# Performance work log

Hardware: AMD Instinct MI355X
Metric: run time of the kernel (lower is better)

## Reference

```python
import jax, jax.numpy as jnp
import numpy as np

K = 10          # hardcoded in module (self.K = 10)
H = 26          # neighbors per query point in this run
PAD_H = 28      # layer_ind2neighbor[layer_ind=0]
KP_EXTENT = 1.2 # linear-influence extent


def setup_inputs() -> dict:
    key = jax.random.key(0)
    ks = jax.random.split(key, 6)
    N, Ns, Cin, Cout = 65536, 65536, 64, 128
    q_pts = jax.random.normal(ks[0], (N, 3), jnp.float32)
    s_pts = jax.random.normal(ks[1], (Ns, 3), jnp.float32)
    neighb_inds = jax.random.randint(ks[2], (N, H), 0, Ns)
    x = jax.random.normal(ks[3], (Ns, Cin), jnp.float32)
    # kernel_points_generator: Linear(PAD_H*3 -> K*3)
    gen_W = jax.random.normal(ks[4], (K * 3, PAD_H * 3), jnp.float32) * (1.0 / np.sqrt(PAD_H * 3))
    gen_b = jnp.zeros((K * 3,), jnp.float32)
    # KPConv weights: [K, in, out] (kaiming_uniform in torch; scaled normal here)
    weights = jax.random.normal(ks[5], (K, Cin, Cout), jnp.float32) * (1.0 / np.sqrt(Cin))
    return {"q_pts": q_pts, "s_pts": s_pts, "x": x,
            "gen_W": gen_W, "gen_b": gen_b, "weights": weights,
            "neighb_inds": neighb_inds}


def _kpconv(q_pts, s_pts, x, gen_W, gen_b, weights, neighb_inds):
    N = q_pts.shape[0]
    # shadow support point far away (index Ns)
    s_pad = jnp.concatenate([s_pts, jnp.full((1, 3), 1e6, s_pts.dtype)], axis=0)
    neighbors = s_pad[neighb_inds] - q_pts[:, None, :]                          # [N,H,3]
    # generative kernel points: pad neighbor list with -1 up to PAD_H, run linear
    padded = jnp.concatenate(
        [neighbors, jnp.full((N, PAD_H - H, 3), -1.0, neighbors.dtype)], axis=1)
    kp = (padded.reshape(N, -1) @ gen_W.T + gen_b).reshape(N, 1, K, 3)          # [N,1,K,3]
    diff = neighbors[:, :, None, :] - kp                                        # [N,H,K,3]
    sq_d = jnp.sum(diff * diff, axis=3)                                         # [N,H,K]
    # KP_influence == 'linear'
    all_w = jnp.maximum(1.0 - jnp.sqrt(sq_d) / KP_EXTENT, 0.0)
    all_w = jnp.swapaxes(all_w, 1, 2)                                           # [N,K,H]
    # shadow feature row (zeros) at index Ns
    x_pad = jnp.concatenate([x, jnp.zeros((1, x.shape[1]), x.dtype)], axis=0)
    neighb_x = x_pad[neighb_inds]                                               # [N,H,Cin]
    weighted = jnp.einsum('nkh,nhi->nki', all_w, neighb_x)                      # [N,K,Cin]
    return jnp.einsum('nki,kio->no', weighted, weights)                         # [N,Cout]


def reference(q_pts, s_pts, x, gen_W, gen_b, weights, neighb_inds):
    return _kpconv(q_pts, s_pts, x, gen_W, gen_b, weights, neighb_inds)
```

## Files before the change

### kernel.cpp

```cpp
#include <hip/hip_runtime.h>
#include <stdint.h>

#define N_Q   65536
#define N_S   65536
#define NB_H  26
#define PAD_H 28
#define KP    10
#define CIN   64
#define COUT  128
#define MT    16
#define BM    16

typedef unsigned short u16x8  __attribute__((ext_vector_type(8)));
typedef float          f32x4  __attribute__((ext_vector_type(4)));
typedef _Float16       f16x8  __attribute__((ext_vector_type(8)));
typedef _Float16       f16x2  __attribute__((ext_vector_type(2)));
typedef unsigned int   u32x4  __attribute__((ext_vector_type(4)));
typedef unsigned int   u32x2  __attribute__((ext_vector_type(2)));

#define CVT_BLOCKS 2049
#define PACK_BLOCKS 40

static __device__ __forceinline__ unsigned short f2h(float f) {
  return __builtin_bit_cast(unsigned short, (_Float16)f);
}

static __device__ __forceinline__ unsigned int pkrtz_u32(float a, float b) {
  return __builtin_bit_cast(unsigned int, __builtin_amdgcn_cvt_pkrtz(a, b));
}

static __device__ __forceinline__ float fdot2u(unsigned int a, unsigned int b, float c) {
#if __has_builtin(__builtin_amdgcn_fdot2)
  return __builtin_amdgcn_fdot2(__builtin_bit_cast(f16x2, a),
                                __builtin_bit_cast(f16x2, b), c, false);
#else
  f16x2 ha = __builtin_bit_cast(f16x2, a), hb = __builtin_bit_cast(f16x2, b);
  return c + (float)ha[0] * (float)hb[0] + (float)ha[1] * (float)hb[1];
#endif
}

__global__ void prep_kernel(const float* __restrict__ x,
                            const float* __restrict__ w,
                            unsigned short* __restrict__ xh,
                            unsigned short* __restrict__ bp) {
  if (blockIdx.x < CVT_BLOCKS) {
    long t = (long)blockIdx.x * blockDim.x + threadIdx.x;
    long off = t * 8;
    if (off >= (long)(N_S + 1) * CIN) return;
    u16x8 o;
    if (off < (long)N_S * CIN) {
      f32x4 a = *(const f32x4*)(x + off);
      f32x4 b = *(const f32x4*)(x + off + 4);
      o[0] = f2h(a[0]); o[1] = f2h(a[1]); o[2] = f2h(a[2]); o[3] = f2h(a[3]);
      o[4] = f2h(b[0]); o[5] = f2h(b[1]); o[6] = f2h(b[2]); o[7] = f2h(b[3]);
    } else {
      o = (u16x8)0;
    }
    *(u16x8*)(xh + off) = o;
  } else {
    int t = (blockIdx.x - CVT_BLOCKS) * blockDim.x + threadIdx.x;
    if (t >= 8 * 20 * 64) return;
    int lane = t & 63;
    int frag = t >> 6;
    int ks = frag % 20;
    int ct = frag / 20;
    int row0 = ks * 32 + (lane >> 4) * 8;
    int col  = ct * 16 + (lane & 15);
    u16x8 o;
    #pragma unroll
    for (int j = 0; j < 8; ++j) o[j] = f2h(w[(row0 + j) * COUT + col]);
    *(u16x8*)(bp + (long)t * 8) = o;
  }
}

#define NBR(m, c)    (((float*)smem)[(m) * 80 + (c)])
#define KPQ(m, r)    (((float*)(smem + 5120))[(m) * 30 + (r)])
#define AW(m, hp, k) (((unsigned int*)(smem + 20480))[((m) * 13 + (hp)) * 12 + (k)])
#define INDX(m, h)   (((int*)(smem + 30464))[(m) * 26 + (h)])

__global__ void __launch_bounds__(256, 5)
kpconv_fused(const float* __restrict__ q_pts, const float* __restrict__ s_pts,
             const float* __restrict__ gen_W, const float* __restrict__ gen_b,
             const int* __restrict__ inds, const unsigned short* __restrict__ xh,
             const unsigned short* __restrict__ bp, float* __restrict__ out) {

  __shared__ char smem[32128] __attribute__((aligned(16)));
  unsigned short* sA = (unsigned short*)smem;

  const int  tid  = threadIdx.x;
  const int  lane = tid & 63;
  const int  wv   = tid >> 6;
  const int  m0   = wv * 4;
  const long row0 = (long)blockIdx.x * BM;

  #pragma unroll
  for (int it = 0; it < 2; ++it) {
    int idx = it * 64 + lane;
    if (idx < 4 * NB_H) {
      int m = m0 + idx / NB_H;
      int h = idx % NB_H;
      int n = (int)row0 + m;
      int ind = inds[n * NB_H + h];
      INDX(m, h) = ind;
      float sx, sy, sz;
      if ((unsigned)ind < (unsigned)N_S) {
        sx = s_pts[ind * 3 + 0]; sy = s_pts[ind * 3 + 1]; sz = s_pts[ind * 3 + 2];
      } else {
        sx = 1e6f; sy = 1e6f; sz = 1e6f;
      }
      NBR(m, h * 3 + 0) = sx - q_pts[n * 3 + 0];
      NBR(m, h * 3 + 1) = sy - q_pts[n * 3 + 1];
      NBR(m, h * 3 + 2) = sz - q_pts[n * 3 + 2];
    }
  }
  if (lane < 8) NBR(m0 + (lane >> 1), 78 + (lane & 1)) = -1.0f;
  asm volatile("s_waitcnt lgkmcnt(0)" ::: "memory");

  const int il = lane & 31;
  const int g2 = lane >> 5;
  const int i0 = il * 2;
  const int rA = m0 + g2, rB = m0 + 2 + g2;

  unsigned int xrA[NB_H];
  #pragma unroll
  for (int h = 0; h < NB_H; ++h)
    xrA[h] = *(const unsigned int*)(xh + (long)INDX(rA, h) * CIN + i0);

  #pragma unroll
  for (int it = 0; it < 2; ++it) {
    int idx = it * 64 + lane;
    if (idx < 4 * 30) {
      int m = m0 + idx / 30;
      int r = idx % 30;
      const float* Wr = gen_W + r * (PAD_H * 3);
      const f32x4* W4 = (const f32x4*)Wr;
      const f32x4* N4 = (const f32x4*)&NBR(m, 0);
      f32x4 accv = {0.f, 0.f, 0.f, 0.f};
      #pragma unroll
      for (int j = 0; j < 20; ++j) accv += W4[j] * N4[j];
      KPQ(m, r) = gen_b[r] - (Wr[80] + Wr[81] + Wr[82] + Wr[83])
                + accv[0] + accv[1] + accv[2] + accv[3];
    }
  }
  asm volatile("s_waitcnt lgkmcnt(0)" ::: "memory");

  for (int it = 0; it < 9; ++it) {
    int idx = it * 64 + lane;
    if (idx < 4 * 13 * KP) {
      int k  = idx % KP;
      int t  = idx / KP;
      int m  = m0 + (t & 3);
      int hp = t >> 2;
      float kx = KPQ(m, k * 3 + 0), ky = KPQ(m, k * 3 + 1), kz = KPQ(m, k * 3 + 2);
      int h0 = hp * 2;
      float dx0 = NBR(m, h0 * 3 + 0) - kx;
      float dy0 = NBR(m, h0 * 3 + 1) - ky;
      float dz0 = NBR(m, h0 * 3 + 2) - kz;
      float w0 = fmaxf(1.0f - sqrtf(dx0 * dx0 + dy0 * dy0 + dz0 * dz0) * (1.0f / 1.2f), 0.0f);
      float dx1 = NBR(m, h0 * 3 + 3) - kx;
      float dy1 = NBR(m, h0 * 3 + 4) - ky;
      float dz1 = NBR(m, h0 * 3 + 5) - kz;
      float w1 = fmaxf(1.0f - sqrtf(dx1 * dx1 + dy1 * dy1 + dz1 * dz1) * (1.0f / 1.2f), 0.0f);
      AW(m, hp, k) = pkrtz_u32(w0, w1);
    }
  }
  asm volatile("s_waitcnt lgkmcnt(0)" ::: "memory");
  __builtin_amdgcn_s_barrier();
  asm volatile("" ::: "memory");

  unsigned int xrB[NB_H];
  #pragma unroll
  for (int h = 0; h < NB_H; ++h)
    xrB[h] = *(const unsigned int*)(xh + (long)INDX(rB, h) * CIN + i0);

  const int kq  = (il & 15) >> 2;
  const int qhi = il >> 4;
  const int j2  = (2 * il) & 7;
  const int swz = (kq << 3) ^ (qhi << 5);

#define ROW_COMPUTE(RR, XR)                                                   \
  {                                                                           \
    float acc0[KP], acc1[KP];                                                 \
    _Pragma("unroll")                                                         \
    for (int k = 0; k < KP; ++k) { acc0[k] = 0.f; acc1[k] = 0.f; }            \
    _Pragma("unroll")                                                         \
    for (int p = 0; p < 13; ++p) {                                            \
      unsigned int r0 = XR[2 * p], r1 = XR[2 * p + 1];                        \
      unsigned int p0 = __builtin_amdgcn_perm(r1, r0, 0x05040100u);           \
      unsigned int p1 = __builtin_amdgcn_perm(r1, r0, 0x07060302u);           \
      unsigned int wr[KP];                                                    \
      *(u32x4*)&wr[0] = *(const u32x4*)&AW(RR, p, 0);                         \
      *(u32x4*)&wr[4] = *(const u32x4*)&AW(RR, p, 4);                         \
      *(u32x2*)&wr[8] = *(const u32x2*)&AW(RR, p, 8);                         \
      _Pragma("unroll")                                                       \
      for (int k = 0; k < KP; ++k) {                                          \
        acc0[k] = fdot2u(wr[k], p0, acc0[k]);                                 \
        acc1[k] = fdot2u(wr[k], p1, acc1[k]);                                 \
      }                                                                       \
    }                                                                         \
    const int hb = (((kq * 16 + (RR)) * 8 + j2) ^ swz) + qhi * 512;           \
    _Pragma("unroll")                                                         \
    for (int k = 0; k < KP; ++k)                                              \
      *(unsigned int*)(sA + k * 1024 + hb) = pkrtz_u32(acc0[k], acc1[k]);     \
  }

  ROW_COMPUTE(rA, xrA)
  ROW_COMPUTE(rB, xrB)
#undef ROW_COMPUTE

  const int ct0 = wv * 2, ct1 = ct0 + 1;
  u16x8 pb0[4], pb1[4];
  #pragma unroll
  for (int d = 0; d < 4; ++d) {
    pb0[d] = *(const u16x8*)(bp + (long)((ct0 * 20 + d) * 64 + lane) * 8);
    pb1[d] = *(const u16x8*)(bp + (long)((ct1 * 20 + d) * 64 + lane) * 8);
  }

  asm volatile("s_waitcnt lgkmcnt(0)" ::: "memory");
  __builtin_amdgcn_s_barrier();
  asm volatile("" ::: "memory");

  {
    const int a0 = (lane * 8) ^ ((lane >> 4) << 3);

    f32x4 acc[2];
    acc[0] = (f32x4){0.f, 0.f, 0.f, 0.f};
    acc[1] = (f32x4){0.f, 0.f, 0.f, 0.f};

    #pragma unroll
    for (int ks = 0; ks < 20; ++ks) {
      f16x8 b0 = __builtin_bit_cast(f16x8, pb0[ks & 3]);
      f16x8 b1 = __builtin_bit_cast(f16x8, pb1[ks & 3]);
      if (ks + 4 < 20) {
        pb0[ks & 3] = *(const u16x8*)(bp + (long)((ct0 * 20 + ks + 4) * 64 + lane) * 8);
        pb1[ks & 3] = *(const u16x8*)(bp + (long)((ct1 * 20 + ks + 4) * 64 + lane) * 8);
      }
      u16x8 au = *(const u16x8*)&sA[ks * 512 + (a0 ^ ((ks & 1) << 5))];
      f16x8 a = __builtin_bit_cast(f16x8, au);
      acc[0] = __builtin_amdgcn_mfma_f32_16x16x32_f16(a, b0, acc[0], 0, 0, 0);
      acc[1] = __builtin_amdgcn_mfma_f32_16x16x32_f16(a, b1, acc[1], 0, 0, 0);
    }

    const int col   = lane & 15;
    const int rbase = (lane >> 4) * 4;
    #pragma unroll
    for (int r = 0; r < 4; ++r) {
      long row = row0 + rbase + r;
      __builtin_nontemporal_store(acc[0][r], &out[row * COUT + ct0 * 16 + col]);
      __builtin_nontemporal_store(acc[1][r], &out[row * COUT + ct1 * 16 + col]);
    }
  }
}

extern "C" void kernel_launch(void* const* d_in, const int* in_sizes, int n_in,
                              void* d_out, int out_size, void* d_ws, size_t ws_size,
                              hipStream_t stream) {
  const float* q_pts = (const float*)d_in[0];
  const float* s_pts = (const float*)d_in[1];
  const float* x     = (const float*)d_in[2];
  const float* gen_W = (const float*)d_in[3];
  const float* gen_b = (const float*)d_in[4];
  const float* wts   = (const float*)d_in[5];
  const int*   inds  = (const int*)d_in[6];
  float* out = (float*)d_out;

  unsigned short* xh = (unsigned short*)d_ws;
  unsigned short* bp = xh + (size_t)(N_S + 1) * CIN;

  prep_kernel<<<CVT_BLOCKS + PACK_BLOCKS, 256, 0, stream>>>(x, wts, xh, bp);
  kpconv_fused<<<N_Q / BM, 256, 0, stream>>>(q_pts, s_pts, gen_W, gen_b,
                                             inds, xh, bp, out);
}
```

Baseline: 184.1 us.

## Stream neighbor feature gathers through an 8-slot register ring, interleaving both rows

Before, all 26 neighbor feature words for row A were gathered before the kernel-point stage, and all 26 for row B after the barrier. Now only the first 8 per row are prefetched, and the rest are loaded inside the weighted-sum loop through a rotating 8-entry register buffer. Rows A and B are also computed together in one loop. The aim is to cut register pressure and raise occupancy while overlapping gather latency with the dot-product work. The cost is that loads now sit closer to their use, which can expose memory latency, and the doubled accumulators for the two rows add registers of their own.

```diff
diff --git a/kernel.cpp b/kernel.cpp
--- a/kernel.cpp
+++ b/kernel.cpp
@@ -120,11 +120,12 @@
   const int g2 = lane >> 5;
   const int i0 = il * 2;
   const int rA = m0 + g2, rB = m0 + 2 + g2;
-
-  unsigned int xrA[NB_H];
-  #pragma unroll
-  for (int h = 0; h < NB_H; ++h)
+  unsigned int xrA[8], xrB[8];
+  #pragma unroll
+  for (int h = 0; h < 8; ++h) {
     xrA[h] = *(const unsigned int*)(xh + (long)INDX(rA, h) * CIN + i0);
+    xrB[h] = *(const unsigned int*)(xh + (long)INDX(rB, h) * CIN + i0);
+  }
 
   #pragma unroll
   for (int it = 0; it < 2; ++it) {
@@ -168,45 +169,57 @@
   __builtin_amdgcn_s_barrier();
   asm volatile("" ::: "memory");
 
-  unsigned int xrB[NB_H];
-  #pragma unroll
-  for (int h = 0; h < NB_H; ++h)
-    xrB[h] = *(const unsigned int*)(xh + (long)INDX(rB, h) * CIN + i0);
-
-  const int kq  = (il & 15) >> 2;
-  const int qhi = il >> 4;
-  const int j2  = (2 * il) & 7;
-  const int swz = (kq << 3) ^ (qhi << 5);
-
-#define ROW_COMPUTE(RR, XR)                                                   \
-  {                                                                           \
-    float acc0[KP], acc1[KP];                                                 \
-    _Pragma("unroll")                                                         \
-    for (int k = 0; k < KP; ++k) { acc0[k] = 0.f; acc1[k] = 0.f; }            \
-    _Pragma("unroll")                                                         \
-    for (int p = 0; p < 13; ++p) {                                            \
-      unsigned int r0 = XR[2 * p], r1 = XR[2 * p + 1];                        \
-      unsigned int p0 = __builtin_amdgcn_perm(r1, r0, 0x05040100u);           \
-      unsigned int p1 = __builtin_amdgcn_perm(r1, r0, 0x07060302u);           \
-      unsigned int wr[KP];                                                    \
-      *(u32x4*)&wr[0] = *(const u32x4*)&AW(RR, p, 0);                         \
-      *(u32x4*)&wr[4] = *(const u32x4*)&AW(RR, p, 4);                         \
-      *(u32x2*)&wr[8] = *(const u32x2*)&AW(RR, p, 8);                         \
-      _Pragma("unroll")                                                       \
-      for (int k = 0; k < KP; ++k) {                                          \
-        acc0[k] = fdot2u(wr[k], p0, acc0[k]);                                 \
-        acc1[k] = fdot2u(wr[k], p1, acc1[k]);                                 \
-      }                                                                       \
-    }                                                                         \
-    const int hb = (((kq * 16 + (RR)) * 8 + j2) ^ swz) + qhi * 512;           \
-    _Pragma("unroll")                                                         \
-    for (int k = 0; k < KP; ++k)                                              \
-      *(unsigned int*)(sA + k * 1024 + hb) = pkrtz_u32(acc0[k], acc1[k]);     \
-  }
-
-  ROW_COMPUTE(rA, xrA)
-  ROW_COMPUTE(rB, xrB)
-#undef ROW_COMPUTE
+  {
+    float a0A[KP], a1A[KP], a0B[KP], a1B[KP];
+    #pragma unroll
+    for (int k = 0; k < KP; ++k) { a0A[k] = 0.f; a1A[k] = 0.f; a0B[k] = 0.f; a1B[k] = 0.f; }
+
+    #pragma unroll
+    for (int p = 0; p < 13; ++p) {
+      unsigned int r0A = xrA[(2 * p) & 7], r1A = xrA[(2 * p + 1) & 7];
+      unsigned int r0B = xrB[(2 * p) & 7], r1B = xrB[(2 * p + 1) & 7];
+      if (2 * p + 8 < NB_H) {
+        xrA[(2 * p) & 7] = *(const unsigned int*)(xh + (long)INDX(rA, 2 * p + 8) * CIN + i0);
+        xrB[(2 * p) & 7] = *(const unsigned int*)(xh + (long)INDX(rB, 2 * p + 8) * CIN + i0);
+      }
+      if (2 * p + 9 < NB_H) {
+        xrA[(2 * p + 1) & 7] = *(const unsigned int*)(xh + (long)INDX(rA, 2 * p + 9) * CIN + i0);
+        xrB[(2 * p + 1) & 7] = *(const unsigned int*)(xh + (long)INDX(rB, 2 * p + 9) * CIN + i0);
+      }
+      unsigned int p0A = __builtin_amdgcn_perm(r1A, r0A, 0x05040100u);
+      unsigned int p1A = __builtin_amdgcn_perm(r1A, r0A, 0x07060302u);
+      unsigned int p0B = __builtin_amdgcn_perm(r1B, r0B, 0x05040100u);
+      unsigned int p1B = __builtin_amdgcn_perm(r1B, r0B, 0x07060302u);
+
+      unsigned int wA[KP], wB[KP];
+      *(u32x4*)&wA[0] = *(const u32x4*)&AW(rA, p, 0);
+      *(u32x4*)&wA[4] = *(const u32x4*)&AW(rA, p, 4);
+      *(u32x2*)&wA[8] = *(const u32x2*)&AW(rA, p, 8);
+      *(u32x4*)&wB[0] = *(const u32x4*)&AW(rB, p, 0);
+      *(u32x4*)&wB[4] = *(const u32x4*)&AW(rB, p, 4);
+      *(u32x2*)&wB[8] = *(const u32x2*)&AW(rB, p, 8);
+
+      #pragma unroll
+      for (int k = 0; k < KP; ++k) {
+        a0A[k] = fdot2u(wA[k], p0A, a0A[k]);
+        a1A[k] = fdot2u(wA[k], p1A, a1A[k]);
+        a0B[k] = fdot2u(wB[k], p0B, a0B[k]);
+        a1B[k] = fdot2u(wB[k], p1B, a1B[k]);
+      }
+    }
+
+    const int kq  = (il & 15) >> 2;
+    const int qhi = il >> 4;
+    const int j2  = (2 * il) & 7;
+    const int swz = (kq << 3) ^ (qhi << 5);
+    const int hbA = (((kq * 16 + rA) * 8 + j2) ^ swz) + qhi * 512;
+    const int hbB = (((kq * 16 + rB) * 8 + j2) ^ swz) + qhi * 512;
+    #pragma unroll
+    for (int k = 0; k < KP; ++k) {
+      *(unsigned int*)(sA + k * 1024 + hbA) = pkrtz_u32(a0A[k], a1A[k]);
+      *(unsigned int*)(sA + k * 1024 + hbB) = pkrtz_u32(a0B[k], a1B[k]);
+    }
+  }
 
   const int ct0 = wv * 2, ct1 = ct0 + 1;
   u16x8 pb0[4], pb1[4];
```

New measurement: 172.0 us. 6.6% less time.

## Use 512-thread blocks with one row per wave and rolling gather prefetch

Applied to the files above, without the earlier changes.

Doubles the workgroup to 8 waves so each wave handles two query rows (one per half-wave) instead of four, and one output column tile in the MFMA stage instead of two. The per-lane feature gather changes from two 26-register preloads to an 8-deep rolling prefetch ring inside the dot-product loop. The aim is lower register pressure and more waves in flight to hide the latency of the irregular gathers. The cost is more barrier participants per block, and the shallower prefetch may expose more of the gather latency.

```diff
diff --git a/kernel.cpp b/kernel.cpp
--- a/kernel.cpp
+++ b/kernel.cpp
@@ -78,7 +78,7 @@
 #define AW(m, hp, k) (((unsigned int*)(smem + 20480))[((m) * 13 + (hp)) * 12 + (k)])
 #define INDX(m, h)   (((int*)(smem + 30464))[(m) * 26 + (h)])
 
-__global__ void __launch_bounds__(256, 5)
+__global__ void __launch_bounds__(512, 6)
 kpconv_fused(const float* __restrict__ q_pts, const float* __restrict__ s_pts,
              const float* __restrict__ gen_W, const float* __restrict__ gen_b,
              const int* __restrict__ inds, const unsigned short* __restrict__ xh,
@@ -90,67 +90,59 @@
   const int  tid  = threadIdx.x;
   const int  lane = tid & 63;
   const int  wv   = tid >> 6;
-  const int  m0   = wv * 4;
+  const int  m0   = wv * 2;
   const long row0 = (long)blockIdx.x * BM;
 
+  if (lane < 2 * NB_H) {
+    int m = m0 + lane / NB_H;
+    int h = lane % NB_H;
+    int n = (int)row0 + m;
+    int ind = inds[n * NB_H + h];
+    INDX(m, h) = ind;
+    float sx, sy, sz;
+    if ((unsigned)ind < (unsigned)N_S) {
+      sx = s_pts[ind * 3 + 0]; sy = s_pts[ind * 3 + 1]; sz = s_pts[ind * 3 + 2];
+    } else {
+      sx = 1e6f; sy = 1e6f; sz = 1e6f;
+    }
+    NBR(m, h * 3 + 0) = sx - q_pts[n * 3 + 0];
+    NBR(m, h * 3 + 1) = sy - q_pts[n * 3 + 1];
+    NBR(m, h * 3 + 2) = sz - q_pts[n * 3 + 2];
+  }
+  if (lane < 4) NBR(m0 + (lane >> 1), 78 + (lane & 1)) = -1.0f;
+  asm volatile("s_waitcnt lgkmcnt(0)" ::: "memory");
+
+  const int il   = lane & 31;
+  const int g2   = lane >> 5;
+  const int i0   = il * 2;
+  const int rowc = m0 + g2;
+  unsigned int xr[8];
   #pragma unroll
-  for (int it = 0; it < 2; ++it) {
+  for (int h = 0; h < 8; ++h)
+    xr[h] = *(const unsigned int*)(xh + (long)INDX(rowc, h) * CIN + i0);
+
+  if (lane < 2 * 30) {
+    int m = m0 + lane / 30;
+    int r = lane % 30;
+    const float* Wr = gen_W + r * (PAD_H * 3);
+    const f32x4* W4 = (const f32x4*)Wr;
+    const f32x4* N4 = (const f32x4*)&NBR(m, 0);
+    f32x4 accv = {0.f, 0.f, 0.f, 0.f};
+    #pragma unroll
+    for (int j = 0; j < 20; ++j) accv += W4[j] * N4[j];
+    KPQ(m, r) = gen_b[r] - (Wr[80] + Wr[81] + Wr[82] + Wr[83])
+              + accv[0] + accv[1] + accv[2] + accv[3];
+  }
+  asm volatile("s_waitcnt lgkmcnt(0)" ::: "memory");
+
+  #pragma unroll
+  for (int it = 0; it < 5; ++it) {
     int idx = it * 64 + lane;
-    if (idx < 4 * NB_H) {
-      int m = m0 + idx / NB_H;
-      int h = idx % NB_H;
-      int n = (int)row0 + m;
-      int ind = inds[n * NB_H + h];
-      INDX(m, h) = ind;
-      float sx, sy, sz;
-      if ((unsigned)ind < (unsigned)N_S) {
-        sx = s_pts[ind * 3 + 0]; sy = s_pts[ind * 3 + 1]; sz = s_pts[ind * 3 + 2];
-      } else {
-        sx = 1e6f; sy = 1e6f; sz = 1e6f;
-      }
-      NBR(m, h * 3 + 0) = sx - q_pts[n * 3 + 0];
-      NBR(m, h * 3 + 1) = sy - q_pts[n * 3 + 1];
-      NBR(m, h * 3 + 2) = sz - q_pts[n * 3 + 2];
-    }
-  }
-  if (lane < 8) NBR(m0 + (lane >> 1), 78 + (lane & 1)) = -1.0f;
-  asm volatile("s_waitcnt lgkmcnt(0)" ::: "memory");
-
-  const int il = lane & 31;
-  const int g2 = lane >> 5;
-  const int i0 = il * 2;
-  const int rA = m0 + g2, rB = m0 + 2 + g2;
-
-  unsigned int xrA[NB_H];
-  #pragma unroll
-  for (int h = 0; h < NB_H; ++h)
-    xrA[h] = *(const unsigned int*)(xh + (long)INDX(rA, h) * CIN + i0);
-
-  #pragma unroll
-  for (int it = 0; it < 2; ++it) {
-    int idx = it * 64 + lane;
-    if (idx < 4 * 30) {
-      int m = m0 + idx / 30;
-      int r = idx % 30;
-      const float* Wr = gen_W + r * (PAD_H * 3);
-      const f32x4* W4 = (const f32x4*)Wr;
-      const f32x4* N4 = (const f32x4*)&NBR(m, 0);
-      f32x4 accv = {0.f, 0.f, 0.f, 0.f};
-      #pragma unroll
-      for (int j = 0; j < 20; ++j) accv += W4[j] * N4[j];
-      KPQ(m, r) = gen_b[r] - (Wr[80] + Wr[81] + Wr[82] + Wr[83])
-                + accv[0] + accv[1] + accv[2] + accv[3];
-    }
-  }
-  asm volatile("s_waitcnt lgkmcnt(0)" ::: "memory");
-
-  for (int it = 0; it < 9; ++it) {
-    int idx = it * 64 + lane;
-    if (idx < 4 * 13 * KP) {
+    if (idx < 2 * 13 * KP) {
       int k  = idx % KP;
       int t  = idx / KP;
-      int m  = m0 + (t & 3);
-      int hp = t >> 2;
+      int m  = m0 + (t & 1);
+      int hp = t >> 1;
       float kx = KPQ(m, k * 3 + 0), ky = KPQ(m, k * 3 + 1), kz = KPQ(m, k * 3 + 2);
       int h0 = hp * 2;
       float dx0 = NBR(m, h0 * 3 + 0) - kx;
@@ -168,53 +160,49 @@
   __builtin_amdgcn_s_barrier();
   asm volatile("" ::: "memory");
 
-  unsigned int xrB[NB_H];
+  {
+    float acc0[KP], acc1[KP];
+    #pragma unroll
+    for (int k = 0; k < KP; ++k) { acc0[k] = 0.f; acc1[k] = 0.f; }
+
+    #pragma unroll
+    for (int p = 0; p < 13; ++p) {
+      unsigned int r0 = xr[(2 * p) & 7];
+      unsigned int r1 = xr[(2 * p + 1) & 7];
+      if (2 * p + 8 < NB_H)
+        xr[(2 * p) & 7] = *(const unsigned int*)(xh + (long)INDX(rowc, 2 * p + 8) * CIN + i0);
+      if (2 * p + 9 < NB_H)
+        xr[(2 * p + 1) & 7] = *(const unsigned int*)(xh + (long)INDX(rowc, 2 * p + 9) * CIN + i0);
+      unsigned int p0 = __builtin_amdgcn_perm(r1, r0, 0x05040100u);
+      unsigned int p1 = __builtin_amdgcn_perm(r1, r0, 0x07060302u);
+
+      unsigned int wr[KP];
+      *(u32x4*)&wr[0] = *(const u32x4*)&AW(rowc, p, 0);
+      *(u32x4*)&wr[4] = *(const u32x4*)&AW(rowc, p, 4);
+      *(u32x2*)&wr[8] = *(const u32x2*)&AW(rowc, p, 8);
+
+      #pragma unroll
+      for (int k = 0; k < KP; ++k) {
+        acc0[k] = fdot2u(wr[k], p0, acc0[k]);
+        acc1[k] = fdot2u(wr[k], p1, acc1[k]);
+      }
+    }
+
+    const int kq  = (il & 15) >> 2;
+    const int qhi = il >> 4;
+    const int j2  = (2 * il) & 7;
+    const int swz = (kq << 3) ^ (qhi << 5);
+    const int hb  = (((kq * 16 + rowc) * 8 + j2) ^ swz) + qhi * 512;
+    #pragma unroll
+    for (int k = 0; k < KP; ++k)
+      *(unsigned int*)(sA + k * 1024 + hb) = pkrtz_u32(acc0[k], acc1[k]);
+  }
+
+  const int ct = wv;
+  u16x8 pb[4];
   #pragma unroll
-  for (int h = 0; h < NB_H; ++h)
-    xrB[h] = *(const unsigned int*)(xh + (long)INDX(rB, h) * CIN + i0);
-
-  const int kq  = (il & 15) >> 2;
-  const int qhi = il >> 4;
-  const int j2  = (2 * il) & 7;
-  const int swz = (kq << 3) ^ (qhi << 5);
-
-#define ROW_COMPUTE(RR, XR)                                                   \
-  {                                                                           \
-    float acc0[KP], acc1[KP];                                                 \
-    _Pragma("unroll")                                                         \
-    for (int k = 0; k < KP; ++k) { acc0[k] = 0.f; acc1[k] = 0.f; }            \
-    _Pragma("unroll")                                                         \
-    for (int p = 0; p < 13; ++p) {                                            \
-      unsigned int r0 = XR[2 * p], r1 = XR[2 * p + 1];                        \
-      unsigned int p0 = __builtin_amdgcn_perm(r1, r0, 0x05040100u);           \
-      unsigned int p1 = __builtin_amdgcn_perm(r1, r0, 0x07060302u);           \
-      unsigned int wr[KP];                                                    \
-      *(u32x4*)&wr[0] = *(const u32x4*)&AW(RR, p, 0);                         \
-      *(u32x4*)&wr[4] = *(const u32x4*)&AW(RR, p, 4);                         \
-      *(u32x2*)&wr[8] = *(const u32x2*)&AW(RR, p, 8);                         \
-      _Pragma("unroll")                                                       \
-      for (int k = 0; k < KP; ++k) {                                          \
-        acc0[k] = fdot2u(wr[k], p0, acc0[k]);                                 \
-        acc1[k] = fdot2u(wr[k], p1, acc1[k]);                                 \
-      }                                                                       \
-    }                                                                         \
-    const int hb = (((kq * 16 + (RR)) * 8 + j2) ^ swz) + qhi * 512;           \
-    _Pragma("unroll")                                                         \
-    for (int k = 0; k < KP; ++k)                                              \
-      *(unsigned int*)(sA + k * 1024 + hb) = pkrtz_u32(acc0[k], acc1[k]);     \
-  }
-
-  ROW_COMPUTE(rA, xrA)
-  ROW_COMPUTE(rB, xrB)
-#undef ROW_COMPUTE
-
-  const int ct0 = wv * 2, ct1 = ct0 + 1;
-  u16x8 pb0[4], pb1[4];
-  #pragma unroll
-  for (int d = 0; d < 4; ++d) {
-    pb0[d] = *(const u16x8*)(bp + (long)((ct0 * 20 + d) * 64 + lane) * 8);
-    pb1[d] = *(const u16x8*)(bp + (long)((ct1 * 20 + d) * 64 + lane) * 8);
-  }
+  for (int d = 0; d < 4; ++d)
+    pb[d] = *(const u16x8*)(bp + (long)((ct * 20 + d) * 64 + lane) * 8);
 
   asm volatile("s_waitcnt lgkmcnt(0)" ::: "memory");
   __builtin_amdgcn_s_barrier();
@@ -223,22 +211,16 @@
   {
     const int a0 = (lane * 8) ^ ((lane >> 4) << 3);
 
-    f32x4 acc[2];
-    acc[0] = (f32x4){0.f, 0.f, 0.f, 0.f};
-    acc[1] = (f32x4){0.f, 0.f, 0.f, 0.f};
+    f32x4 acc = (f32x4){0.f, 0.f, 0.f, 0.f};
 
     #pragma unroll
     for (int ks = 0; ks < 20; ++ks) {
-      f16x8 b0 = __builtin_bit_cast(f16x8, pb0[ks & 3]);
-      f16x8 b1 = __builtin_bit_cast(f16x8, pb1[ks & 3]);
-      if (ks + 4 < 20) {
-        pb0[ks & 3] = *(const u16x8*)(bp + (long)((ct0 * 20 + ks + 4) * 64 + lane) * 8);
-        pb1[ks & 3] = *(const u16x8*)(bp + (long)((ct1 * 20 + ks + 4) * 64 + lane) * 8);
-      }
+      f16x8 b = __builtin_bit_cast(f16x8, pb[ks & 3]);
+      if (ks + 4 < 20)
+        pb[ks & 3] = *(const u16x8*)(bp + (long)((ct * 20 + ks + 4) * 64 + lane) * 8);
       u16x8 au = *(const u16x8*)&sA[ks * 512 + (a0 ^ ((ks & 1) << 5))];
       f16x8 a = __builtin_bit_cast(f16x8, au);
-      acc[0] = __builtin_amdgcn_mfma_f32_16x16x32_f16(a, b0, acc[0], 0, 0, 0);
-      acc[1] = __builtin_amdgcn_mfma_f32_16x16x32_f16(a, b1, acc[1], 0, 0, 0);
+      acc = __builtin_amdgcn_mfma_f32_16x16x32_f16(a, b, acc, 0, 0, 0);
     }
 
     const int col   = lane & 15;
@@ -246,8 +228,7 @@
     #pragma unroll
     for (int r = 0; r < 4; ++r) {
       long row = row0 + rbase + r;
-      __builtin_nontemporal_store(acc[0][r], &out[row * COUT + ct0 * 16 + col]);
-      __builtin_nontemporal_store(acc[1][r], &out[row * COUT + ct1 * 16 + col]);
+      __builtin_nontemporal_store(acc[r], &out[row * COUT + ct * 16 + col]);
     }
   }
 }
@@ -268,6 +249,6 @@
   unsigned short* bp = xh + (size_t)(N_S + 1) * CIN;
 
   prep_kernel<<<CVT_BLOCKS + PACK_BLOCKS, 256, 0, stream>>>(x, wts, xh, bp);
-  kpconv_fused<<<N_Q / BM, 256, 0, stream>>>(q_pts, s_pts, gen_W, gen_b,
+  kpconv_fused<<<N_Q / BM, 512, 0, stream>>>(q_pts, s_pts, gen_W, gen_b,
                                              inds, xh, bp, out);
 }
```

Measured after the change: 167.3 us. 1.1x faster.
